# Optimization experiments

Hardware: AMD Instinct MI355X
Metric: run time of the kernel (lower is better)

## Reference

```python
import jax, jax.numpy as jnp
import numpy as np

H, W = 5, 11          # fixed spatial map from ConvLSTM2D((5,11), ...)
P = H * W             # 55 pixels; 1x1 convs are per-pixel linear layers
HC = 64               # hidden channels
IC = 2                # input channels
FC_DIMS = [2 * HC * P, 3400, 1000, 500, 50]  # 7040 -> 3400 -> 1000 -> 500 -> 50


def setup_inputs() -> dict:
    key = jax.random.key(0)
    ks = jax.random.split(key, 24)
    B, T = 32, 256
    s = 0.05
    d = {}
    d["x1"] = jax.random.normal(ks[0], (B, T, IC, H, W), jnp.float32)
    d["x2"] = jax.random.normal(ks[1], (B, T, IC, H, W), jnp.float32)
    # ConvLSTM cell params: 1x1 convs fused into (in, 4*HC) matrices, gate order i,f,o,g
    d["wx1"] = jax.random.normal(ks[2], (IC, 4 * HC), jnp.float32) * s
    d["wh1"] = jax.random.normal(ks[3], (HC, 4 * HC), jnp.float32) * s
    d["bx1"] = jax.random.normal(ks[4], (4 * HC,), jnp.float32) * s
    d["bh1"] = jax.random.normal(ks[5], (4 * HC,), jnp.float32) * s
    d["wx2"] = jax.random.normal(ks[6], (IC, 4 * HC), jnp.float32) * s
    d["wh2"] = jax.random.normal(ks[7], (HC, 4 * HC), jnp.float32) * s
    d["bx2"] = jax.random.normal(ks[8], (4 * HC,), jnp.float32) * s
    d["bh2"] = jax.random.normal(ks[9], (4 * HC,), jnp.float32) * s
    # FC stack (stored as (in,out) so y = x @ W + b, equivalent to torch Linear)
    for i in range(4):
        fan_in, fan_out = FC_DIMS[i], FC_DIMS[i + 1]
        lim = 1.0 / np.sqrt(fan_in)
        d[f"fw{i+2}"] = jax.random.uniform(ks[10 + 2 * i], (fan_in, fan_out), jnp.float32, -lim, lim)
        d[f"fb{i+2}"] = jax.random.uniform(ks[11 + 2 * i], (fan_out,), jnp.float32, -lim, lim)
    return d


def _cell_step(h, c, gx, wh, bh):
    # gx: (B,P,4*HC) precomputed x contribution; h,c: (B,P,HC)
    g = gx + h @ wh + bh
    i, f, o, gg = jnp.split(g, 4, axis=-1)
    c = jax.nn.sigmoid(f) * c + jax.nn.sigmoid(i) * jnp.tanh(gg)
    h = jax.nn.sigmoid(o) * jnp.tanh(c)
    return h, c


def _sub_forward(x, wx1, wh1, bx1, bh1, wx2, wh2, bx2, bh2,
                 fw2, fb2, fw3, fb3, fw4, fb4, fw5, fb5):
    B, T = x.shape[0], x.shape[1]
    # (B,T,C,H,W) -> (B,T,P,C): pixels become a batch dim for the 1x1 convs
    xs = x.transpose(0, 1, 3, 4, 2).reshape(B, T, P, IC)
    # Precompute all input-to-gate projections once (big batched GEMM)
    gx1 = jnp.einsum('btpc,cd->btpd', xs, wx1) + bx1            # cell1: forward in time
    gx2 = jnp.einsum('btpc,cd->btpd', xs[:, ::-1], wx2) + bx2   # cell2: reversed in time
    h0 = jnp.zeros((B, P, HC), x.dtype)

    def step(carry, g):
        h1, c1, h2, c2 = carry
        g1, g2 = g
        h1, c1 = _cell_step(h1, c1, g1, wh1, bh1)
        h2, c2 = _cell_step(h2, c2, g2, wh2, bh2)
        return (h1, c1, h2, c2), None

    (h1, _, h2, _), _ = jax.lax.scan(
        step, (h0, h0, h0, h0),
        (gx1.transpose(1, 0, 2, 3), gx2.transpose(1, 0, 2, 3)))

    # torch.cat((h1,h2),1) on (B,HC,H,W) then flatten -> channel-major layout
    out = jnp.concatenate([h1.transpose(0, 2, 1), h2.transpose(0, 2, 1)], axis=1).reshape(B, -1)
    out = out @ fw2 + fb2
    out = out @ fw3 + fb3
    out = out @ fw4 + fb4
    out = out @ fw5 + fb5
    return out


def reference(x1, x2, wx1, wh1, bx1, bh1, wx2, wh2, bx2, bh2,
              fw2, fb2, fw3, fb3, fw4, fb4, fw5, fb5):
    args = (wx1, wh1, bx1, bh1, wx2, wh2, bx2, bh2,
            fw2, fb2, fw3, fb3, fw4, fb4, fw5, fb5)
    out1 = _sub_forward(x1, *args)
    out2 = _sub_forward(x2, *args)
    return (out1, out2)
```

## Files before the change

kernel.cpp:

```cpp
#include <hip/hip_runtime.h>


#define T_STEPS 256
#define PIX 55
#define MT 16
#define TILES 110
#define LOG2E 1.4426950408889634f
#define FC_GRP 16

typedef float f32x4 __attribute__((ext_vector_type(4)));
typedef __bf16 bf16x8 __attribute__((ext_vector_type(8)));
typedef __bf16 bf16x4 __attribute__((ext_vector_type(4)));

__global__ __launch_bounds__(256) void lstm_kernel(
    const float* __restrict__ x1, const float* __restrict__ x2,
    const float* __restrict__ wx1, const float* __restrict__ wh1,
    const float* __restrict__ bx1, const float* __restrict__ bh1,
    const float* __restrict__ wx2, const float* __restrict__ wh2,
    const float* __restrict__ bx2, const float* __restrict__ bh2,
    float* __restrict__ feat)
{
    int bid  = blockIdx.x;
    int tile = bid % TILES;
    int cc   = bid / TILES;
    int sub  = cc >> 1, cell = cc & 1;
    const float* x  = sub  ? x2  : x1;
    const float* wx = cell ? wx2 : wx1;
    const float* wh = cell ? wh2 : wh1;
    const float* bx = cell ? bx2 : bx1;
    const float* bh = cell ? bh2 : bh1;

    int tid  = threadIdx.x;
    int w    = tid >> 6;
    int l    = tid & 63;
    int quad = l >> 4;
    int c16  = l & 15;

    __shared__ float xl[MT * 514];
    __shared__ __align__(16) __bf16 hb[2][2][MT][72];

    {
        int seq0 = tile * MT;
        for (int i = 0; i < 32; ++i) {
            int idx = tid + 256 * i;
            int m = idx >> 9;
            int tc = idx & 511;
            int t = tc >> 1, c = tc & 1;
            int seq = seq0 + m;
            int b = seq / PIX, p = seq % PIX;
            xl[m * 514 + tc] = x[((b * T_STEPS + t) * 2 + c) * PIX + p];
        }
    }
    {
        __bf16* hz = &hb[0][0][0][0];
        for (int i = tid; i < 2 * 2 * MT * 72; i += 256) hz[i] = (__bf16)0.0f;
    }

    bf16x8 Whi[4][2], Wlo[4][2];
    float btot[4][4], wxa[4][4], wxb[4][4];
#pragma unroll
    for (int g = 0; g < 4; ++g) {
        int col = 64 * g + 16 * w + c16;
#pragma unroll
        for (int r = 0; r < 4; ++r) {
            int u = 64 * g + 16 * w + 4 * quad + r;
            btot[g][r] = bx[u] + bh[u];
            wxa[g][r]  = wx[u];
            wxb[g][r]  = wx[256 + u];
        }
#pragma unroll
        for (int q = 0; q < 2; ++q) {
#pragma unroll
            for (int j = 0; j < 8; ++j) {
                int k = 32 * q + 8 * quad + j;
                float wv = wh[k * 256 + col];
                __bf16 hi = (__bf16)wv;
                Whi[g][q][j] = hi;
                Wlo[g][q][j] = (__bf16)(wv - (float)hi);
            }
        }
    }

    float cst[4]  = {0.f, 0.f, 0.f, 0.f};
    float hfin[4] = {0.f, 0.f, 0.f, 0.f};

    __syncthreads();
    float2 xv = *(const float2*)&xl[c16 * 514 + (cell ? (T_STEPS - 1) : 0) * 2];

#pragma unroll 2
    for (int t = 0; t < T_STEPS; ++t) {
        int rb = t & 1, wb = rb ^ 1;

        bf16x8 Bh[2], Bl[2];
#pragma unroll
        for (int q = 0; q < 2; ++q) {
            Bh[q] = *(const bf16x8*)&hb[rb][0][c16][32 * q + 8 * quad];
            Bl[q] = *(const bf16x8*)&hb[rb][1][c16][32 * q + 8 * quad];
        }

        f32x4 acc[4];
#pragma unroll
        for (int g = 0; g < 4; ++g) {
#pragma unroll
            for (int r = 0; r < 4; ++r)
                acc[g][r] = fmaf(xv.y, wxb[g][r], fmaf(xv.x, wxa[g][r], btot[g][r]));
        }
#pragma unroll
        for (int g = 0; g < 4; ++g)
            acc[g] = __builtin_amdgcn_mfma_f32_16x16x32_bf16(Whi[g][0], Bh[0], acc[g], 0, 0, 0);
#pragma unroll
        for (int g = 0; g < 4; ++g)
            acc[g] = __builtin_amdgcn_mfma_f32_16x16x32_bf16(Whi[g][1], Bh[1], acc[g], 0, 0, 0);
#pragma unroll
        for (int g = 0; g < 4; ++g)
            acc[g] = __builtin_amdgcn_mfma_f32_16x16x32_bf16(Wlo[g][0], Bh[0], acc[g], 0, 0, 0);
#pragma unroll
        for (int g = 0; g < 4; ++g)
            acc[g] = __builtin_amdgcn_mfma_f32_16x16x32_bf16(Wlo[g][1], Bh[1], acc[g], 0, 0, 0);
#pragma unroll
        for (int g = 0; g < 4; ++g)
            acc[g] = __builtin_amdgcn_mfma_f32_16x16x32_bf16(Whi[g][0], Bl[0], acc[g], 0, 0, 0);
#pragma unroll
        for (int g = 0; g < 4; ++g)
            acc[g] = __builtin_amdgcn_mfma_f32_16x16x32_bf16(Whi[g][1], Bl[1], acc[g], 0, 0, 0);

        float ei[4], ef[4], eo[4], eg[4];
#pragma unroll
        for (int r = 0; r < 4; ++r) {
            ei[r] = __builtin_amdgcn_exp2f(-LOG2E * acc[0][r]);
            ef[r] = __builtin_amdgcn_exp2f(-LOG2E * acc[1][r]);
            eo[r] = __builtin_amdgcn_exp2f(-LOG2E * acc[2][r]);
            eg[r] = __builtin_amdgcn_exp2f(-2.0f * LOG2E * acc[3][r]);
        }

        bf16x4 ph, pl;
#pragma unroll
        for (int r = 0; r < 4; ++r) {
            float sf  = __builtin_amdgcn_rcpf(1.0f + ef[r]);
            float itg = (1.0f - eg[r]) * __builtin_amdgcn_rcpf((1.0f + ei[r]) * (1.0f + eg[r]));
            float c   = fmaf(sf, cst[r], itg);
            cst[r] = c;
            float ec = __builtin_amdgcn_exp2f(-2.0f * LOG2E * c);
            float h  = (1.0f - ec) * __builtin_amdgcn_rcpf((1.0f + eo[r]) * (1.0f + ec));
            hfin[r] = h;
            __bf16 hi = (__bf16)h;
            ph[r] = hi;
            pl[r] = (__bf16)(h - (float)hi);
        }
        *(bf16x4*)&hb[wb][0][c16][16 * w + 4 * quad] = ph;
        *(bf16x4*)&hb[wb][1][c16][16 * w + 4 * quad] = pl;

        {
            int txn = (cell ? (T_STEPS - 2 - t) : (t + 1)) & 255;
            xv = *(const float2*)&xl[c16 * 514 + txn * 2];
        }
        __syncthreads();
    }

    {
        int seq = tile * MT + c16;
        int b = seq / PIX, p = seq % PIX;
#pragma unroll
        for (int r = 0; r < 4; ++r) {
            int u = 16 * w + 4 * quad + r;
            feat[(size_t)(sub * 32 + b) * 7040 + (cell * 64 + u) * PIX + p] = hfin[r];
        }
    }
}

__global__ __launch_bounds__(256) void fc_init(
    const float* __restrict__ b2, const float* __restrict__ b3,
    const float* __restrict__ b4, const float* __restrict__ b5,
    float* __restrict__ t1, float* __restrict__ t2,
    float* __restrict__ t3, float* __restrict__ o)
{
    int i = blockIdx.x * 256 + threadIdx.x;
    const int n1 = 64 * 3400, n2 = 64 * 1000, n3 = 64 * 500, n4 = 64 * 50;
    if (i < n1) { t1[i] = b2[i % 3400]; return; }
    i -= n1;
    if (i < n2) { t2[i] = b3[i % 1000]; return; }
    i -= n2;
    if (i < n3) { t3[i] = b4[i % 500]; return; }
    i -= n3;
    if (i < n4) { o[i] = b5[i % 50]; }
}

__global__ __launch_bounds__(256) void fc_gemm(const float* __restrict__ A,
                                               const float* __restrict__ W,
                                               float* __restrict__ out,
                                               int K, int N, int kchunk) {
    int tid  = threadIdx.x;
    int l    = tid & 63;
    int row0 = __builtin_amdgcn_readfirstlane((tid >> 6) * 16);
    int k0   = blockIdx.y * kchunk;
    int kend = min(K, k0 + kchunk);

    int n  = blockIdx.x * 64 + l;
    int ne = min(n, N - 1);

    const float* ar = A + (size_t)row0 * K;
    const float* wp = W + ne;

    float acc[16];
#pragma unroll
    for (int i = 0; i < 16; ++i) acc[i] = 0.0f;

    int ks = k0;
    for (; ks + FC_GRP <= kend; ks += FC_GRP) {
        float wbuf[FC_GRP];
#pragma unroll
        for (int j = 0; j < FC_GRP; ++j)
            wbuf[j] = wp[(size_t)(ks + j) * N];
#pragma unroll
        for (int j = 0; j < FC_GRP; ++j) {
#pragma unroll
            for (int m = 0; m < 16; ++m)
                acc[m] = fmaf(ar[(size_t)m * K + ks + j], wbuf[j], acc[m]);
        }
    }
    for (; ks < kend; ++ks) {
        float wvv = wp[(size_t)ks * N];
#pragma unroll
        for (int m = 0; m < 16; ++m)
            acc[m] = fmaf(ar[(size_t)m * K + ks], wvv, acc[m]);
    }

    if (n < N) {
        float* pr = out + n;
#pragma unroll
        for (int i = 0; i < 16; ++i)
            unsafeAtomicAdd(&pr[(size_t)(row0 + i) * N], acc[i]);
    }
}

extern "C" void kernel_launch(void* const* d_in, const int* in_sizes, int n_in,
                              void* d_out, int out_size, void* d_ws, size_t ws_size,
                              hipStream_t stream) {
    const float* x1  = (const float*)d_in[0];
    const float* x2  = (const float*)d_in[1];
    const float* wx1 = (const float*)d_in[2];
    const float* wh1 = (const float*)d_in[3];
    const float* bx1 = (const float*)d_in[4];
    const float* bh1 = (const float*)d_in[5];
    const float* wx2 = (const float*)d_in[6];
    const float* wh2 = (const float*)d_in[7];
    const float* bx2 = (const float*)d_in[8];
    const float* bh2 = (const float*)d_in[9];
    const float* fw2 = (const float*)d_in[10];
    const float* fb2 = (const float*)d_in[11];
    const float* fw3 = (const float*)d_in[12];
    const float* fb3 = (const float*)d_in[13];
    const float* fw4 = (const float*)d_in[14];
    const float* fb4 = (const float*)d_in[15];
    const float* fw5 = (const float*)d_in[16];
    const float* fb5 = (const float*)d_in[17];

    char* ws = (char*)d_ws;
    float* feat = (float*)ws;
    float* t1   = feat + (size_t)64 * 7040;
    float* t2   = t1   + (size_t)64 * 3400;
    float* t3   = t2   + (size_t)64 * 1000;
    float* o    = (float*)d_out;

    fc_init<<<dim3(1238), dim3(256), 0, stream>>>(fb2, fb3, fb4, fb5, t1, t2, t3, o);

    lstm_kernel<<<dim3(440), dim3(256), 0, stream>>>(
        x1, x2, wx1, wh1, bx1, bh1, wx2, wh2, bx2, bh2, feat);

    fc_gemm<<<dim3(54, 44), dim3(256), 0, stream>>>(feat, fw2, t1, 7040, 3400, 160);
    fc_gemm<<<dim3(16, 107), dim3(256), 0, stream>>>(t1, fw3, t2, 3400, 1000, 32);
    fc_gemm<<<dim3(8, 63), dim3(256), 0, stream>>>(t2, fw4, t3, 1000, 500, 16);
    fc_gemm<<<dim3(1, 32), dim3(256), 0, stream>>>(t3, fw5, o, 500, 50, 16);
}
```

Baseline: 632.8 us.

## Use split-bf16 MFMA for FC GEMMs with LDS-staged activations

```diff
diff --git a/kernel.cpp b/kernel.cpp
--- a/kernel.cpp
+++ b/kernel.cpp
@@ -6,7 +6,8 @@
 #define MT 16
 #define TILES 110
 #define LOG2E 1.4426950408889634f
-#define FC_GRP 16
+#define FCM_STAGE 128
+#define FCM_PAD 8
 
 typedef float f32x4 __attribute__((ext_vector_type(4)));
 typedef __bf16 bf16x8 __attribute__((ext_vector_type(8)));
@@ -189,47 +190,75 @@
                                                const float* __restrict__ W,
                                                float* __restrict__ out,
                                                int K, int N, int kchunk) {
+    __shared__ __align__(16) __bf16 alh[64][FCM_STAGE + FCM_PAD];
+    __shared__ __align__(16) __bf16 all[64][FCM_STAGE + FCM_PAD];
+
     int tid  = threadIdx.x;
     int l    = tid & 63;
-    int row0 = __builtin_amdgcn_readfirstlane((tid >> 6) * 16);
+    int wv   = tid >> 6;
+    int quad = l >> 4;
+    int c16  = l & 15;
+
     int k0   = blockIdx.y * kchunk;
     int kend = min(K, k0 + kchunk);
 
-    int n  = blockIdx.x * 64 + l;
-    int ne = min(n, N - 1);
-
-    const float* ar = A + (size_t)row0 * K;
-    const float* wp = W + ne;
-
-    float acc[16];
-#pragma unroll
-    for (int i = 0; i < 16; ++i) acc[i] = 0.0f;
-
-    int ks = k0;
-    for (; ks + FC_GRP <= kend; ks += FC_GRP) {
-        float wbuf[FC_GRP];
-#pragma unroll
-        for (int j = 0; j < FC_GRP; ++j)
-            wbuf[j] = wp[(size_t)(ks + j) * N];
-#pragma unroll
-        for (int j = 0; j < FC_GRP; ++j) {
-#pragma unroll
-            for (int m = 0; m < 16; ++m)
-                acc[m] = fmaf(ar[(size_t)m * K + ks + j], wbuf[j], acc[m]);
-        }
-    }
-    for (; ks < kend; ++ks) {
-        float wvv = wp[(size_t)ks * N];
-#pragma unroll
-        for (int m = 0; m < 16; ++m)
-            acc[m] = fmaf(ar[(size_t)m * K + ks], wvv, acc[m]);
+    int n  = blockIdx.x * 64 + 16 * wv + c16;
+    int nc = min(n, N - 1);
+
+    f32x4 acc[4];
+#pragma unroll
+    for (int mt = 0; mt < 4; ++mt) acc[mt] = (f32x4){0.f, 0.f, 0.f, 0.f};
+
+    for (int ks = k0; ks < kend; ks += FCM_STAGE) {
+        int kcur = min(FCM_STAGE, kend - ks);
+        __syncthreads();
+#pragma unroll
+        for (int i = 0; i < 32; ++i) {
+            int idx = tid + 256 * i;
+            int m = idx >> 7, kc = idx & 127;
+            float v = (kc < kcur) ? A[(size_t)m * K + ks + kc] : 0.0f;
+            __bf16 hi = (__bf16)v;
+            alh[m][kc] = hi;
+            all[m][kc] = (__bf16)(v - (float)hi);
+        }
+        __syncthreads();
+
+        int nslab = (kcur + 31) >> 5;
+        for (int s = 0; s < nslab; ++s) {
+            bf16x8 wh, wl;
+#pragma unroll
+            for (int e = 0; e < 8; ++e) {
+                int kr = ks + 32 * s + 8 * quad + e;
+                float wval = W[(size_t)min(kr, K - 1) * N + nc];
+                __bf16 hi = (__bf16)wval;
+                wh[e] = hi;
+                wl[e] = (__bf16)(wval - (float)hi);
+            }
+            int ko = 32 * s + 8 * quad;
+            bf16x8 ah[4], alo[4];
+#pragma unroll
+            for (int mt = 0; mt < 4; ++mt) {
+                ah[mt]  = *(const bf16x8*)&alh[c16 + 16 * mt][ko];
+                alo[mt] = *(const bf16x8*)&all[c16 + 16 * mt][ko];
+            }
+#pragma unroll
+            for (int mt = 0; mt < 4; ++mt)
+                acc[mt] = __builtin_amdgcn_mfma_f32_16x16x32_bf16(ah[mt], wh, acc[mt], 0, 0, 0);
+#pragma unroll
+            for (int mt = 0; mt < 4; ++mt)
+                acc[mt] = __builtin_amdgcn_mfma_f32_16x16x32_bf16(alo[mt], wh, acc[mt], 0, 0, 0);
+#pragma unroll
+            for (int mt = 0; mt < 4; ++mt)
+                acc[mt] = __builtin_amdgcn_mfma_f32_16x16x32_bf16(ah[mt], wl, acc[mt], 0, 0, 0);
+        }
     }
 
     if (n < N) {
-        float* pr = out + n;
-#pragma unroll
-        for (int i = 0; i < 16; ++i)
-            unsafeAtomicAdd(&pr[(size_t)(row0 + i) * N], acc[i]);
+#pragma unroll
+        for (int mt = 0; mt < 4; ++mt)
+#pragma unroll
+            for (int r = 0; r < 4; ++r)
+                unsafeAtomicAdd(&out[(size_t)(16 * mt + 4 * quad + r) * N + n], acc[mt][r]);
     }
 }
 
@@ -267,8 +296,8 @@
     lstm_kernel<<<dim3(440), dim3(256), 0, stream>>>(
         x1, x2, wx1, wh1, bx1, bh1, wx2, wh2, bx2, bh2, feat);
 
-    fc_gemm<<<dim3(54, 44), dim3(256), 0, stream>>>(feat, fw2, t1, 7040, 3400, 160);
-    fc_gemm<<<dim3(16, 107), dim3(256), 0, stream>>>(t1, fw3, t2, 3400, 1000, 32);
-    fc_gemm<<<dim3(8, 63), dim3(256), 0, stream>>>(t2, fw4, t3, 1000, 500, 16);
-    fc_gemm<<<dim3(1, 32), dim3(256), 0, stream>>>(t3, fw5, o, 500, 50, 16);
+    fc_gemm<<<dim3(54, 11), dim3(256), 0, stream>>>(feat, fw2, t1, 7040, 3400, 640);
+    fc_gemm<<<dim3(16, 27), dim3(256), 0, stream>>>(t1, fw3, t2, 3400, 1000, 128);
+    fc_gemm<<<dim3(8, 8), dim3(256), 0, stream>>>(t2, fw4, t3, 1000, 500, 128);
+    fc_gemm<<<dim3(1, 4), dim3(256), 0, stream>>>(t3, fw5, o, 500, 50, 128);
 }
```

Result: faster. 572.4 us (-9.5%).
